# Kernel optimization log

Hardware: AMD Instinct MI355X
Metric: run time of the kernel (lower is better)

## Reference

```python
import jax, jax.numpy as jnp
import numpy as np

NUM_HEADS = 6

def setup_inputs() -> dict:
    key = jax.random.key(0)
    k1, k2, k3, k4 = jax.random.split(key, 4)
    B, T, C = 128, 256, 384
    s = 1.0 / np.sqrt(C)
    return {
        'x': jax.random.normal(k1, (B, T, C), dtype=jnp.float32),
        'Wq': jax.random.normal(k2, (C, C), dtype=jnp.float32) * s,
        'Wk': jax.random.normal(k3, (C, C), dtype=jnp.float32) * s,
        'Wv': jax.random.normal(k4, (C, C), dtype=jnp.float32) * s,
    }

def reference(x, Wq, Wk, Wv):
    B, T, C = x.shape
    H = NUM_HEADS
    d = C // H
    # projections (bias-free Linear), split into heads
    q = (x @ Wq).reshape(B, T, H, d)
    k = (x @ Wk).reshape(B, T, H, d)
    v = (x @ Wv).reshape(B, T, H, d)
    # NOTE: original scales by 1/sqrt(C), not 1/sqrt(head_dim)
    scale = 1.0 / jnp.sqrt(jnp.asarray(C, dtype=x.dtype))
    att = jnp.einsum('bqhd,bkhd->bhqk', q, k) * scale  # [B,H,T,T]
    causal = jnp.tril(jnp.ones((T, T), dtype=bool))
    att = jnp.where(causal, att, -jnp.inf)
    att = jax.nn.softmax(att, axis=-1)
    # dropout is identity in eval/deterministic mode
    out = jnp.einsum('bhqk,bkhd->bqhd', att, v)  # [B,T,H,d]
    return out.reshape(B, T, C)
```

## Files before the change

kernel.cpp:

```cpp
#include <hip/hip_runtime.h>


typedef unsigned short u16;
typedef float f32x4 __attribute__((ext_vector_type(4)));
typedef short s16x8 __attribute__((ext_vector_type(8)));
typedef u16 u16x4 __attribute__((ext_vector_type(4)));

static constexpr int BB = 128;
static constexpr int TT = 256;
static constexpr int CC = 384;
static constexpr int HH = 6;
static constexpr int DD = 64;
static constexpr int MM = BB * TT;

static constexpr size_t WTOFF = 0;
static constexpr size_t XOFF  = (size_t)3 * CC * CC;

static constexpr float CSC = 0.07362242194579907f;

__device__ __forceinline__ u16 f2bf(float f) {
  unsigned u = __float_as_uint(f);
  u += 0x7fffu + ((u >> 16) & 1u);
  return (u16)(u >> 16);
}

__device__ __forceinline__ void g2l16(const u16* g, u16* l) {
  __builtin_amdgcn_global_load_lds(
      (const __attribute__((address_space(1))) u16*)g,
      (__attribute__((address_space(3))) u16*)l, 16, 0, 0);
}

__global__ void prep(const float* __restrict__ X, const float* __restrict__ Wq,
                     const float* __restrict__ Wk, const float* __restrict__ Wv,
                     u16* __restrict__ ws) {
  int bx = blockIdx.x;
  if (bx < 6144) {
    size_t i = (size_t)(bx * 256 + threadIdx.x) * 8;
    f32x4 a0 = *(const f32x4*)(X + i);
    f32x4 a1 = *(const f32x4*)(X + i + 4);
    s16x8 ab;
#pragma unroll
    for (int j = 0; j < 4; ++j) { ab[j] = (short)f2bf(a0[j]); ab[4 + j] = (short)f2bf(a1[j]); }
    *(s16x8*)(ws + XOFF + i) = ab;
  } else {
    __shared__ u16 Lt[64][66];
    int j = bx - 6144;
    int z = j / 36, t = j % 36, ti = t / 6, tj = t % 6;
    const float* W = (z == 0) ? Wq : (z == 1) ? Wk : Wv;
    const float sc = (z == 0) ? CSC : 1.0f;
    u16* WT = ws + WTOFF + (size_t)z * CC * CC;
    const int rl = threadIdx.x >> 4;
    const int cl = (threadIdx.x & 15) * 4;
#pragma unroll
    for (int it = 0; it < 4; ++it) {
      int r = it * 16 + rl;
      f32x4 v = *(const f32x4*)(W + (size_t)(ti * 64 + r) * CC + tj * 64 + cl);
#pragma unroll
      for (int q = 0; q < 4; ++q) Lt[r][cl + q] = f2bf(v[q] * sc);
    }
    __syncthreads();
#pragma unroll
    for (int it = 0; it < 4; ++it) {
      int n = it * 16 + rl;
      u16x4 o;
#pragma unroll
      for (int q = 0; q < 4; ++q) o[q] = Lt[cl + q][n];
      *(u16x4*)(WT + (size_t)(tj * 64 + n) * CC + ti * 64 + cl) = o;
    }
  }
}

__global__ __launch_bounds__(512, 2) void fused(const u16* __restrict__ ws,
                                                float* __restrict__ out) {
  const int bid = blockIdx.x;
  const int xc = bid & 7;
  const int g5 = bid >> 3;
  const int b = xc * 16 + g5 / 6;
  const int h = g5 % 6;

  __shared__ u16 R1[256][64];
  __shared__ u16 R2[16384];
  __shared__ u16 Ks[256][64];
  __shared__ u16 VTs[64][256];

  const int tid = threadIdx.x;
  const int lane = tid & 63;
  const int w = tid >> 6;
  const int quad = lane >> 4;
  const int col = lane & 15;

  const u16* Xg = ws + XOFF + (size_t)b * TT * CC;
  const u16* Wg = ws + WTOFF;
  u16* Wst = R2;

  const int rl = lane >> 3;
  const int gb = (lane & 7) ^ rl;

  const int wm = (w >> 1) * 64;
  const int wn = (w & 1) * 96;

  auto stage = [&](int kt) {
#pragma unroll
    for (int i = 0; i < 4; ++i) {
      int r0 = w * 32 + i * 8;
      g2l16(Xg + (size_t)(r0 + rl) * CC + kt * 64 + gb * 8, &R1[r0][0]);
    }
#pragma unroll
    for (int i = 0; i < 3; ++i) {
      int r0 = w * 24 + i * 8;
      int rr = r0 + rl;
      int z = rr >> 6, nn = rr & 63;
      g2l16(Wg + (size_t)(z * CC + h * DD + nn) * CC + kt * 64 + gb * 8,
            Wst + r0 * 64);
    }
  };

  f32x4 acc[4][6] = {};

  stage(0);
  __syncthreads();

  for (int kt = 0; kt < 6; ++kt) {
    s16x8 af[4][2], bf[6][2];
#pragma unroll
    for (int mt = 0; mt < 4; ++mt)
#pragma unroll
      for (int ks = 0; ks < 2; ++ks)
        af[mt][ks] = *(const s16x8*)(&R1[wm + mt * 16 + col]
                                        [(((ks * 4 + quad) ^ (col & 7)) * 8)]);
#pragma unroll
    for (int nt = 0; nt < 6; ++nt)
#pragma unroll
      for (int ks = 0; ks < 2; ++ks)
        bf[nt][ks] = *(const s16x8*)(Wst + (wn + nt * 16 + col) * 64 +
                                     (((ks * 4 + quad) ^ (col & 7)) * 8));

    __syncthreads();
    if (kt < 5) stage(kt + 1);

    __builtin_amdgcn_s_setprio(1);
#pragma unroll
    for (int ks = 0; ks < 2; ++ks)
#pragma unroll
      for (int mt = 0; mt < 4; ++mt)
#pragma unroll
        for (int nt = 0; nt < 6; ++nt)
          acc[mt][nt] = __builtin_amdgcn_mfma_f32_16x16x32_bf16(
              af[mt][ks], bf[nt][ks], acc[mt][nt], 0, 0, 0);
    __builtin_amdgcn_s_setprio(0);

    if (kt < 5) __syncthreads();
  }

#pragma unroll
  for (int mt = 0; mt < 4; ++mt) {
    int tokb = wm + mt * 16 + quad * 4;
#pragma unroll
    for (int nt = 0; nt < 6; ++nt) {
      int gn = wn + nt * 16 + col;
      if (gn < 128) {
        u16* dst = (gn < 64) ? &R1[0][0] : &Ks[0][0];
        int d = gn & 63;
#pragma unroll
        for (int r = 0; r < 4; ++r) {
          int tok = tokb + r;
          dst[tok * 64 + (d ^ ((tok & 7) << 3))] = f2bf(acc[mt][nt][r]);
        }
      } else {
        int d = gn - 128;
        uint2 pk;
        pk.x = (unsigned)f2bf(acc[mt][nt][0]) | ((unsigned)f2bf(acc[mt][nt][1]) << 16);
        pk.y = (unsigned)f2bf(acc[mt][nt][2]) | ((unsigned)f2bf(acc[mt][nt][3]) << 16);
        *(uint2*)((u16*)VTs + d * 256 + (tokb ^ ((d & 15) << 3))) = pk;
      }
    }
  }
  __syncthreads();

  const int g0 = w, g1 = 15 - w;
  const int k0max = g0 >> 2, k1max = g1 >> 2;
  const int qq0 = (g0 & 3) * 16 + col;
  const int qq1 = (g1 & 3) * 16 + col;
  u16* PsA = R2 + w * 2048;
  u16* PsB = PsA + 1024;

  s16x8 qf[2][2];
  {
    int qr0 = g0 * 16 + col, qr1 = g1 * 16 + col;
#pragma unroll
    for (int ks = 0; ks < 2; ++ks) {
      qf[0][ks] = *(const s16x8*)(&R1[qr0][(((ks * 4 + quad) ^ (col & 7)) * 8)]);
      qf[1][ks] = *(const s16x8*)(&R1[qr1][(((ks * 4 + quad) ^ (col & 7)) * 8)]);
    }
  }

  f32x4 o[2][4] = {};
  float mst[2] = {-1.0e30f, -1.0e30f}, lst[2] = {0.0f, 0.0f};

  auto sm = [&](f32x4 (&s)[4], bool diag, int qq, float& m, float& l,
                unsigned (&pk)[4][2]) -> float {
    float rmax = -1.0e30f;
#pragma unroll
    for (int nt = 0; nt < 4; ++nt)
#pragma unroll
      for (int r = 0; r < 4; ++r) {
        float t = s[nt][r];
        if (diag && (nt * 16 + quad * 4 + r) > qq) t = -1.0e30f;
        s[nt][r] = t;
        rmax = fmaxf(rmax, t);
      }
    rmax = fmaxf(rmax, __shfl_xor(rmax, 16));
    rmax = fmaxf(rmax, __shfl_xor(rmax, 32));
    float mn = fmaxf(m, rmax);
    float alpha = exp2f(m - mn);
    m = mn;
    float lsum = 0.0f;
#pragma unroll
    for (int nt = 0; nt < 4; ++nt) {
      float p0 = exp2f(s[nt][0] - mn), p1 = exp2f(s[nt][1] - mn);
      float p2 = exp2f(s[nt][2] - mn), p3 = exp2f(s[nt][3] - mn);
      lsum += (p0 + p1) + (p2 + p3);
      pk[nt][0] = (unsigned)f2bf(p0) | ((unsigned)f2bf(p1) << 16);
      pk[nt][1] = (unsigned)f2bf(p2) | ((unsigned)f2bf(p3) << 16);
    }
    l = l * alpha + lsum;
    return alpha;
  };

  for (int kt = 0; kt <= k1max; ++kt) {
    const bool both = (kt <= k0max);

    s16x8 kf[4][2], vf[4][2];
#pragma unroll
    for (int nt = 0; nt < 4; ++nt)
#pragma unroll
      for (int ks = 0; ks < 2; ++ks) {
        int key = kt * 64 + nt * 16 + col;
        kf[nt][ks] = *(const s16x8*)(&Ks[key][(((ks * 4 + quad) ^ (col & 7)) * 8)]);
        int d = nt * 16 + col;
        vf[nt][ks] = *(const s16x8*)((const u16*)VTs + d * 256 +
                     ((kt * 64 + ks * 32 + quad * 8) ^ ((d & 15) << 3)));
      }

    f32x4 sA[4] = {}, sB[4] = {};
    __builtin_amdgcn_s_setprio(1);
    if (both) {
#pragma unroll
      for (int ks = 0; ks < 2; ++ks)
#pragma unroll
        for (int nt = 0; nt < 4; ++nt)
          sA[nt] = __builtin_amdgcn_mfma_f32_16x16x32_bf16(kf[nt][ks], qf[0][ks],
                                                           sA[nt], 0, 0, 0);
    }
#pragma unroll
    for (int ks = 0; ks < 2; ++ks)
#pragma unroll
      for (int nt = 0; nt < 4; ++nt)
        sB[nt] = __builtin_amdgcn_mfma_f32_16x16x32_bf16(kf[nt][ks], qf[1][ks],
                                                         sB[nt], 0, 0, 0);
    __builtin_amdgcn_s_setprio(0);

    unsigned pkA[4][2], pkB[4][2];
    float aA = 1.0f, aB;
    if (both) {
      aA = sm(sA, kt == k0max, qq0, mst[0], lst[0], pkA);
#pragma unroll
      for (int nt = 0; nt < 4; ++nt)
        *(uint2*)(PsA + col * 64 + ((nt * 16 + quad * 4) ^ ((col & 7) << 3))) =
            make_uint2(pkA[nt][0], pkA[nt][1]);
    }
    aB = sm(sB, kt == k1max, qq1, mst[1], lst[1], pkB);
#pragma unroll
    for (int nt = 0; nt < 4; ++nt)
      *(uint2*)(PsB + col * 64 + ((nt * 16 + quad * 4) ^ ((col & 7) << 3))) =
          make_uint2(pkB[nt][0], pkB[nt][1]);

    if (both) {
#pragma unroll
      for (int dt = 0; dt < 4; ++dt)
#pragma unroll
        for (int r = 0; r < 4; ++r) o[0][dt][r] *= aA;
    }
#pragma unroll
    for (int dt = 0; dt < 4; ++dt)
#pragma unroll
      for (int r = 0; r < 4; ++r) o[1][dt][r] *= aB;

    asm volatile("s_waitcnt lgkmcnt(0)" ::: "memory");

    s16x8 pfA[2], pfB[2];
    if (both) {
#pragma unroll
      for (int ks = 0; ks < 2; ++ks)
        pfA[ks] = *(const s16x8*)(PsA + col * 64 +
                                  ((ks * 32 + quad * 8) ^ ((col & 7) << 3)));
    }
#pragma unroll
    for (int ks = 0; ks < 2; ++ks)
      pfB[ks] = *(const s16x8*)(PsB + col * 64 +
                                ((ks * 32 + quad * 8) ^ ((col & 7) << 3)));

    __builtin_amdgcn_s_setprio(1);
    if (both) {
#pragma unroll
      for (int ks = 0; ks < 2; ++ks)
#pragma unroll
        for (int dt = 0; dt < 4; ++dt)
          o[0][dt] = __builtin_amdgcn_mfma_f32_16x16x32_bf16(vf[dt][ks], pfA[ks],
                                                             o[0][dt], 0, 0, 0);
    }
#pragma unroll
    for (int ks = 0; ks < 2; ++ks)
#pragma unroll
      for (int dt = 0; dt < 4; ++dt)
        o[1][dt] = __builtin_amdgcn_mfma_f32_16x16x32_bf16(vf[dt][ks], pfB[ks],
                                                           o[1][dt], 0, 0, 0);
    __builtin_amdgcn_s_setprio(0);
  }

#pragma unroll
  for (int gi = 0; gi < 2; ++gi) {
    int g = gi ? g1 : g0;
    float l = lst[gi];
    l += __shfl_xor(l, 16);
    l += __shfl_xor(l, 32);
    float inv = 1.0f / l;
    int q = g * 16 + col;
#pragma unroll
    for (int dt = 0; dt < 4; ++dt) {
      f32x4 res;
#pragma unroll
      for (int r = 0; r < 4; ++r) res[r] = o[gi][dt][r] * inv;
      *(f32x4*)(out + (size_t)(b * TT + q) * CC + h * DD + dt * 16 + quad * 4) = res;
    }
  }
}

extern "C" void kernel_launch(void* const* d_in, const int* in_sizes, int n_in,
                              void* d_out, int out_size, void* d_ws, size_t ws_size,
                              hipStream_t stream) {
  const float* x  = (const float*)d_in[0];
  const float* wq = (const float*)d_in[1];
  const float* wk = (const float*)d_in[2];
  const float* wv = (const float*)d_in[3];
  u16* ws  = (u16*)d_ws;
  float* out = (float*)d_out;

  prep<<<dim3(6144 + 108), 256, 0, stream>>>(x, wq, wk, wv, ws);
  fused<<<dim3(BB * HH), 512, 0, stream>>>(ws, out);
}
```

Measured before the change: 154.9 us.

## Double-buffer projection GEMM staging with two K-tiles per barrier

Shared memory is reorganised into two X and W staging buffers, so the QKV projection loop handles two 64-wide K tiles per iteration and loads the next pair asynchronously after the barrier. This halves the number of block-wide barriers in the projection phase and lets fragment reads of the second buffer overlap with MFMA on the first. After the GEMM the buffers are reused for Q, K and the softmax P scratch. Shared memory use grows slightly (from about 112KB to 128KB), which may limit occupancy with two blocks per CU.

```diff
diff --git a/kernel.cpp b/kernel.cpp
--- a/kernel.cpp
+++ b/kernel.cpp
@@ -78,9 +78,8 @@
   const int b = xc * 16 + g5 / 6;
   const int h = g5 % 6;
 
-  __shared__ u16 R1[256][64];
-  __shared__ u16 R2[16384];
-  __shared__ u16 Ks[256][64];
+  __shared__ u16 X2[2][256][64];
+  __shared__ u16 W2[2][12288];
   __shared__ u16 VTs[64][256];
 
   const int tid = threadIdx.x;
@@ -91,7 +90,6 @@
 
   const u16* Xg = ws + XOFF + (size_t)b * TT * CC;
   const u16* Wg = ws + WTOFF;
-  u16* Wst = R2;
 
   const int rl = lane >> 3;
   const int gb = (lane & 7) ^ rl;
@@ -99,45 +97,49 @@
   const int wm = (w >> 1) * 64;
   const int wn = (w & 1) * 96;
 
-  auto stage = [&](int kt) {
+  auto stage = [&](int t) {
+    u16* Xd = &X2[t & 1][0][0];
+    u16* Wd = &W2[t & 1][0];
 #pragma unroll
     for (int i = 0; i < 4; ++i) {
       int r0 = w * 32 + i * 8;
-      g2l16(Xg + (size_t)(r0 + rl) * CC + kt * 64 + gb * 8, &R1[r0][0]);
+      g2l16(Xg + (size_t)(r0 + rl) * CC + t * 64 + gb * 8, Xd + r0 * 64);
     }
 #pragma unroll
     for (int i = 0; i < 3; ++i) {
       int r0 = w * 24 + i * 8;
       int rr = r0 + rl;
       int z = rr >> 6, nn = rr & 63;
-      g2l16(Wg + (size_t)(z * CC + h * DD + nn) * CC + kt * 64 + gb * 8,
-            Wst + r0 * 64);
+      g2l16(Wg + (size_t)(z * CC + h * DD + nn) * CC + t * 64 + gb * 8,
+            Wd + r0 * 64);
     }
   };
 
+  auto rdfrags = [&](int bufi, s16x8 (&af)[4][2], s16x8 (&bf)[6][2]) {
+#pragma unroll
+    for (int mt = 0; mt < 4; ++mt)
+#pragma unroll
+      for (int ks = 0; ks < 2; ++ks)
+        af[mt][ks] = *(const s16x8*)(&X2[bufi][wm + mt * 16 + col]
+                                        [(((ks * 4 + quad) ^ (col & 7)) * 8)]);
+#pragma unroll
+    for (int nt = 0; nt < 6; ++nt)
+#pragma unroll
+      for (int ks = 0; ks < 2; ++ks)
+        bf[nt][ks] = *(const s16x8*)(&W2[bufi][(wn + nt * 16 + col) * 64 +
+                                              (((ks * 4 + quad) ^ (col & 7)) * 8)]);
+  };
+
   f32x4 acc[4][6] = {};
 
   stage(0);
+  stage(1);
   __syncthreads();
 
-  for (int kt = 0; kt < 6; ++kt) {
+  for (int j = 0; j < 3; ++j) {
     s16x8 af[4][2], bf[6][2];
-#pragma unroll
-    for (int mt = 0; mt < 4; ++mt)
-#pragma unroll
-      for (int ks = 0; ks < 2; ++ks)
-        af[mt][ks] = *(const s16x8*)(&R1[wm + mt * 16 + col]
-                                        [(((ks * 4 + quad) ^ (col & 7)) * 8)]);
-#pragma unroll
-    for (int nt = 0; nt < 6; ++nt)
-#pragma unroll
-      for (int ks = 0; ks < 2; ++ks)
-        bf[nt][ks] = *(const s16x8*)(Wst + (wn + nt * 16 + col) * 64 +
-                                     (((ks * 4 + quad) ^ (col & 7)) * 8));
-
-    __syncthreads();
-    if (kt < 5) stage(kt + 1);
-
+
+    rdfrags(0, af, bf);
     __builtin_amdgcn_s_setprio(1);
 #pragma unroll
     for (int ks = 0; ks < 2; ++ks)
@@ -149,9 +151,27 @@
               af[mt][ks], bf[nt][ks], acc[mt][nt], 0, 0, 0);
     __builtin_amdgcn_s_setprio(0);
 
-    if (kt < 5) __syncthreads();
-  }
-
+    rdfrags(1, af, bf);
+    __syncthreads();
+
+    if (j < 2) { stage(2 * j + 2); stage(2 * j + 3); }
+
+    __builtin_amdgcn_s_setprio(1);
+#pragma unroll
+    for (int ks = 0; ks < 2; ++ks)
+#pragma unroll
+      for (int mt = 0; mt < 4; ++mt)
+#pragma unroll
+        for (int nt = 0; nt < 6; ++nt)
+          acc[mt][nt] = __builtin_amdgcn_mfma_f32_16x16x32_bf16(
+              af[mt][ks], bf[nt][ks], acc[mt][nt], 0, 0, 0);
+    __builtin_amdgcn_s_setprio(0);
+
+    if (j < 2) __syncthreads();
+  }
+
+  u16* Qb  = &X2[0][0][0];
+  u16* KsB = &X2[1][0][0];
 #pragma unroll
   for (int mt = 0; mt < 4; ++mt) {
     int tokb = wm + mt * 16 + quad * 4;
@@ -159,7 +179,7 @@
     for (int nt = 0; nt < 6; ++nt) {
       int gn = wn + nt * 16 + col;
       if (gn < 128) {
-        u16* dst = (gn < 64) ? &R1[0][0] : &Ks[0][0];
+        u16* dst = (gn < 64) ? Qb : KsB;
         int d = gn & 63;
 #pragma unroll
         for (int r = 0; r < 4; ++r) {
@@ -181,7 +201,7 @@
   const int k0max = g0 >> 2, k1max = g1 >> 2;
   const int qq0 = (g0 & 3) * 16 + col;
   const int qq1 = (g1 & 3) * 16 + col;
-  u16* PsA = R2 + w * 2048;
+  u16* PsA = &W2[0][0] + w * 2048;
   u16* PsB = PsA + 1024;
 
   s16x8 qf[2][2];
@@ -189,8 +209,8 @@
     int qr0 = g0 * 16 + col, qr1 = g1 * 16 + col;
 #pragma unroll
     for (int ks = 0; ks < 2; ++ks) {
-      qf[0][ks] = *(const s16x8*)(&R1[qr0][(((ks * 4 + quad) ^ (col & 7)) * 8)]);
-      qf[1][ks] = *(const s16x8*)(&R1[qr1][(((ks * 4 + quad) ^ (col & 7)) * 8)]);
+      qf[0][ks] = *(const s16x8*)(Qb + qr0 * 64 + (((ks * 4 + quad) ^ (col & 7)) * 8));
+      qf[1][ks] = *(const s16x8*)(Qb + qr1 * 64 + (((ks * 4 + quad) ^ (col & 7)) * 8));
     }
   }
 
@@ -236,7 +256,8 @@
 #pragma unroll
       for (int ks = 0; ks < 2; ++ks) {
         int key = kt * 64 + nt * 16 + col;
-        kf[nt][ks] = *(const s16x8*)(&Ks[key][(((ks * 4 + quad) ^ (col & 7)) * 8)]);
+        kf[nt][ks] = *(const s16x8*)(KsB + key * 64 +
+                                     (((ks * 4 + quad) ^ (col & 7)) * 8));
         int d = nt * 16 + col;
         vf[nt][ks] = *(const s16x8*)((const u16*)VTs + d * 256 +
                      ((kt * 64 + ks * 32 + quad * 8) ^ ((d & 15) << 3)));
```

Result: no change. 153.2 us (-1.1%).

## Shrink LDS footprint by spilling V-transpose to global workspace for higher occupancy

Applied to the files above, without the earlier changes.

The four 32KB shared buffers become a single 64KB pool. Q and K reuse the X and W staging regions, and the P scratch reuses the Q region after an added barrier. V-transposed is no longer kept in LDS: it is written to a new global workspace region and read back from global memory (expected to hit L2) in the attention loop. Launch bounds rise from 2 to 4 blocks so more blocks can share a CU and hide latency. The risks are register pressure and spills under the tighter register cap, global-memory latency on the V reads, and the workspace having to be large enough for the extra region.

```diff
diff --git a/kernel.cpp b/kernel.cpp
--- a/kernel.cpp
+++ b/kernel.cpp
@@ -15,6 +15,7 @@
 
 static constexpr size_t WTOFF = 0;
 static constexpr size_t XOFF  = (size_t)3 * CC * CC;
+static constexpr size_t VTOFF = XOFF + (size_t)MM * CC;
 
 static constexpr float CSC = 0.07362242194579907f;
 
@@ -70,7 +71,7 @@
   }
 }
 
-__global__ __launch_bounds__(512, 2) void fused(const u16* __restrict__ ws,
+__global__ __launch_bounds__(512, 4) void fused(u16* __restrict__ ws,
                                                 float* __restrict__ out) {
   const int bid = blockIdx.x;
   const int xc = bid & 7;
@@ -78,10 +79,9 @@
   const int b = xc * 16 + g5 / 6;
   const int h = g5 % 6;
 
-  __shared__ u16 R1[256][64];
-  __shared__ u16 R2[16384];
-  __shared__ u16 Ks[256][64];
-  __shared__ u16 VTs[64][256];
+  __shared__ u16 POOL[32768];
+  u16* Xs  = POOL;
+  u16* Wst = POOL + 16384;
 
   const int tid = threadIdx.x;
   const int lane = tid & 63;
@@ -91,7 +91,7 @@
 
   const u16* Xg = ws + XOFF + (size_t)b * TT * CC;
   const u16* Wg = ws + WTOFF;
-  u16* Wst = R2;
+  u16* VTg = ws + VTOFF + (size_t)(b * HH + h) * DD * TT;
 
   const int rl = lane >> 3;
   const int gb = (lane & 7) ^ rl;
@@ -103,7 +103,7 @@
 #pragma unroll
     for (int i = 0; i < 4; ++i) {
       int r0 = w * 32 + i * 8;
-      g2l16(Xg + (size_t)(r0 + rl) * CC + kt * 64 + gb * 8, &R1[r0][0]);
+      g2l16(Xg + (size_t)(r0 + rl) * CC + kt * 64 + gb * 8, Xs + r0 * 64);
     }
 #pragma unroll
     for (int i = 0; i < 3; ++i) {
@@ -126,8 +126,8 @@
     for (int mt = 0; mt < 4; ++mt)
 #pragma unroll
       for (int ks = 0; ks < 2; ++ks)
-        af[mt][ks] = *(const s16x8*)(&R1[wm + mt * 16 + col]
-                                        [(((ks * 4 + quad) ^ (col & 7)) * 8)]);
+        af[mt][ks] = *(const s16x8*)(Xs + (wm + mt * 16 + col) * 64 +
+                                     (((ks * 4 + quad) ^ (col & 7)) * 8));
 #pragma unroll
     for (int nt = 0; nt < 6; ++nt)
 #pragma unroll
@@ -152,6 +152,8 @@
     if (kt < 5) __syncthreads();
   }
 
+  u16* Qb  = Xs;
+  u16* KsB = Wst;
 #pragma unroll
   for (int mt = 0; mt < 4; ++mt) {
     int tokb = wm + mt * 16 + quad * 4;
@@ -159,7 +161,7 @@
     for (int nt = 0; nt < 6; ++nt) {
       int gn = wn + nt * 16 + col;
       if (gn < 128) {
-        u16* dst = (gn < 64) ? &R1[0][0] : &Ks[0][0];
+        u16* dst = (gn < 64) ? Qb : KsB;
         int d = gn & 63;
 #pragma unroll
         for (int r = 0; r < 4; ++r) {
@@ -171,7 +173,7 @@
         uint2 pk;
         pk.x = (unsigned)f2bf(acc[mt][nt][0]) | ((unsigned)f2bf(acc[mt][nt][1]) << 16);
         pk.y = (unsigned)f2bf(acc[mt][nt][2]) | ((unsigned)f2bf(acc[mt][nt][3]) << 16);
-        *(uint2*)((u16*)VTs + d * 256 + (tokb ^ ((d & 15) << 3))) = pk;
+        *(uint2*)(VTg + d * TT + tokb) = pk;
       }
     }
   }
@@ -181,18 +183,20 @@
   const int k0max = g0 >> 2, k1max = g1 >> 2;
   const int qq0 = (g0 & 3) * 16 + col;
   const int qq1 = (g1 & 3) * 16 + col;
-  u16* PsA = R2 + w * 2048;
-  u16* PsB = PsA + 1024;
 
   s16x8 qf[2][2];
   {
     int qr0 = g0 * 16 + col, qr1 = g1 * 16 + col;
 #pragma unroll
     for (int ks = 0; ks < 2; ++ks) {
-      qf[0][ks] = *(const s16x8*)(&R1[qr0][(((ks * 4 + quad) ^ (col & 7)) * 8)]);
-      qf[1][ks] = *(const s16x8*)(&R1[qr1][(((ks * 4 + quad) ^ (col & 7)) * 8)]);
-    }
-  }
+      qf[0][ks] = *(const s16x8*)(Qb + qr0 * 64 + (((ks * 4 + quad) ^ (col & 7)) * 8));
+      qf[1][ks] = *(const s16x8*)(Qb + qr1 * 64 + (((ks * 4 + quad) ^ (col & 7)) * 8));
+    }
+  }
+  __syncthreads();
+
+  u16* PsA = Qb + w * 2048;
+  u16* PsB = PsA + 1024;
 
   f32x4 o[2][4] = {};
   float mst[2] = {-1.0e30f, -1.0e30f}, lst[2] = {0.0f, 0.0f};
@@ -236,10 +240,10 @@
 #pragma unroll
       for (int ks = 0; ks < 2; ++ks) {
         int key = kt * 64 + nt * 16 + col;
-        kf[nt][ks] = *(const s16x8*)(&Ks[key][(((ks * 4 + quad) ^ (col & 7)) * 8)]);
-        int d = nt * 16 + col;
-        vf[nt][ks] = *(const s16x8*)((const u16*)VTs + d * 256 +
-                     ((kt * 64 + ks * 32 + quad * 8) ^ ((d & 15) << 3)));
+        kf[nt][ks] = *(const s16x8*)(KsB + key * 64 +
+                                     (((ks * 4 + quad) ^ (col & 7)) * 8));
+        vf[nt][ks] = *(const s16x8*)(VTg + (nt * 16 + col) * TT +
+                                     kt * 64 + ks * 32 + quad * 8);
       }
 
     f32x4 sA[4] = {}, sB[4] = {};
```

Measured after the change: 508.7 us. 3.28x slower.
